# Optimization experiments

Hardware: AMD Instinct MI355X
Metric: run time of the kernel (lower is better)

The kernel has to match this reference:

```python
import jax, jax.numpy as jnp
import numpy as np

BS, E = 32, 4096  # BS fixed by repeat_interleave(32) in the source


def setup_inputs() -> dict:
    key = jax.random.key(0)
    ks = jax.random.split(key, 8)
    s = lambda k, shape, scale=0.02: jax.random.normal(k, shape, dtype=jnp.float32) * scale
    return {
        "image_features": jax.random.normal(ks[0], (BS, E), dtype=jnp.float32),
        "text_features": jax.random.normal(ks[1], (BS, E), dtype=jnp.float32),
        # fusion: BN(2E) -> ReLU -> Linear(2E,E)
        "fs_bn_g": jnp.ones((2 * E,), jnp.float32),
        "fs_bn_b": jnp.zeros((2 * E,), jnp.float32),
        "fs_w": s(ks[2], (2 * E, E)),
        "fs_b": jnp.zeros((E,), jnp.float32),
        # gating: Linear(E,E) -> BN -> ReLU -> Linear(E,E) -> Sigmoid
        "gt_w1": s(ks[3], (E, E)),
        "gt_b1": jnp.zeros((E,), jnp.float32),
        "gt_bn_g": jnp.ones((E,), jnp.float32),
        "gt_bn_b": jnp.zeros((E,), jnp.float32),
        "gt_w2": s(ks[4], (E, E)),
        "gt_b2": jnp.zeros((E,), jnp.float32),
        # 3 error-encoding blocks: Linear(E,E/2)->BN->ReLU->Linear(E/2,E)+residual
        "ee_w1": s(ks[5], (3, E, E // 2)),
        "ee_b1": jnp.zeros((3, E // 2), jnp.float32),
        "ee_bn_g": jnp.ones((3, E // 2), jnp.float32),
        "ee_bn_b": jnp.zeros((3, E // 2), jnp.float32),
        "ee_w2": s(ks[6], (3, E // 2, E)),
        "ee_b2": jnp.zeros((3, E), jnp.float32),
        "cell_id": 1,
    }


def _bn(x, g, b, eps=1e-5):
    # training-mode BatchNorm1d: per-call batch statistics (biased variance)
    mu = jnp.mean(x, axis=0, keepdims=True)
    var = jnp.mean((x - mu) ** 2, axis=0, keepdims=True)
    return (x - mu) * jax.lax.rsqrt(var + eps) * g + b


def reference(image_features, text_features, fs_bn_g, fs_bn_b, fs_w, fs_b,
              gt_w1, gt_b1, gt_bn_g, gt_bn_b, gt_w2, gt_b2,
              ee_w1, ee_b1, ee_bn_g, ee_bn_b, ee_w2, ee_b2, cell_id):
    # cell_id != 0 branch: the per-sample Python loop is vectorized with vmap.
    def compose(txt_row):  # txt_row: [E] -> tiled to [BS, E] (repeat_interleave of [1,E])
        t = jnp.broadcast_to(txt_row[None, :], image_features.shape)
        x = jnp.concatenate([image_features, t], axis=1)          # [BS, 2E]
        f = jax.nn.relu(_bn(x, fs_bn_g, fs_bn_b)) @ fs_w + fs_b   # fusion -> [BS, E]
        g = jax.nn.sigmoid(
            jax.nn.relu(_bn(f @ gt_w1 + gt_b1, gt_bn_g, gt_bn_b)) @ gt_w2 + gt_b2
        )                                                          # gating -> [BS, E]
        ff = f
        for i in range(3):  # structurally distinct error-encoding blocks
            h = jax.nn.relu(_bn(ff @ ee_w1[i] + ee_b1[i], ee_bn_g[i], ee_bn_b[i]))
            ff = h @ ee_w2[i] + ee_b2[i] + ff                      # residual
        return image_features * g + ff * (1.0 - g)                # [BS, E]

    return jax.vmap(compose)(text_features)                        # [BS, BS, E]
```

## Files before the change

kernel.cpp:

```cpp
#include <hip/hip_runtime.h>
#include <math.h>

#define EDIM 4096
#define BS 32
#define NT 64
#define KSPLIT 4
#define NWAVES 4
#define BLK 256

__device__ __forceinline__ float relu_f(float x) { return x > 0.f ? x : 0.f; }

__global__ void __launch_bounds__(BLK) prep_kernel(
    const float* __restrict__ img, const float* __restrict__ bng,
    const float* __restrict__ bnb, float* __restrict__ act0,
    float* __restrict__ vvec, int* __restrict__ flag)
{
  int n = blockIdx.x * BLK + threadIdx.x;
  float bv = bnb[EDIM + n];
  float vv = relu_f(bv);
  vvec[n] = vv;
  if (vv != 0.f) atomicOr(flag, 1);

  float s = 0.f, s2 = 0.f;
  for (int r = 0; r < BS; ++r) {
    float x = img[(size_t)r * EDIM + n];
    s += x; s2 += x * x;
  }
  float mean = s * (1.f / BS);
  float var  = s2 * (1.f / BS) - mean * mean;
  float sc = bng[n] * rsqrtf(var + 1e-5f);
  float sh = bnb[n] - mean * sc;
  for (int r = 0; r < BS; ++r) {
    float x = img[(size_t)r * EDIM + n];
    act0[(size_t)n * BS + r] = relu_f(x * sc + sh);
  }
}

__global__ void __launch_bounds__(BLK) mm_stage(
    const float* __restrict__ W, const float* __restrict__ Ain,
    const float* __restrict__ bias,
    const float* __restrict__ bng, const float* __restrict__ bnb,
    const float* __restrict__ res,
    const float* __restrict__ Wlow, const float* __restrict__ vvec,
    const int* __restrict__ flag,
    float* __restrict__ acc, int* __restrict__ counter,
    float* __restrict__ dst,
    int K, int N, int mode)
{
  const int tid  = threadIdx.x;
  const int bx   = blockIdx.x;
  const int tile = bx >> 2;
  const int ks   = bx & (KSPLIT - 1);
  const int wv   = __builtin_amdgcn_readfirstlane(tid >> 6);
  const int lane = tid & 63;
  const int n    = tile * NT + lane;
  const int kchunk = K / (KSPLIT * NWAVES);
  const int k0     = (ks * NWAVES + wv) * kchunk;

  float racc[BS];
#pragma unroll
  for (int r = 0; r < BS; ++r) racc[r] = 0.f;

  const float* wp = W + (size_t)k0 * N + n;
  const float* ap = Ain + (size_t)k0 * BS;

#pragma unroll 4
  for (int k = 0; k < kchunk; ++k) {
    float wval = wp[(size_t)k * N];
    const float* arow = ap + (size_t)k * BS;
#pragma unroll
    for (int r = 0; r < BS; ++r) racc[r] = fmaf(arow[r], wval, racc[r]);
  }

  if (Wlow != nullptr) {
    if (*flag) {
      float cpart = 0.f;
      const float* wl = Wlow + (size_t)k0 * N + n;
      for (int k = 0; k < kchunk; ++k)
        cpart = fmaf(vvec[k0 + k], wl[(size_t)k * N], cpart);
#pragma unroll
      for (int r = 0; r < BS; ++r) racc[r] += cpart;
    }
  }

  __shared__ float sred[NWAVES][NT][BS];
#pragma unroll
  for (int r = 0; r < BS; r += 4)
    *(float4*)&sred[wv][lane][r] = make_float4(racc[r], racc[r+1], racc[r+2], racc[r+3]);
  __syncthreads();

  const int c  = tid >> 2;
  const int rb = (tid & 3) * 8;
  float tot[8];
#pragma unroll
  for (int u = 0; u < 8; ++u)
    tot[u] = sred[0][c][rb+u] + sred[1][c][rb+u] + sred[2][c][rb+u] + sred[3][c][rb+u];

  const int col = tile * NT + c;
  float* ga = acc + (size_t)col * BS + rb;
#pragma unroll
  for (int u = 0; u < 8; ++u) atomicAdd(ga + u, tot[u]);

  __threadfence();
  __syncthreads();
  __shared__ int s_last;
  if (tid == 0) {
    int old = atomicAdd(counter + tile, 1);
    s_last = (old == KSPLIT - 1) ? 1 : 0;
  }
  __syncthreads();
  if (!s_last) return;

  float val[8];
#pragma unroll
  for (int u = 0; u < 8; ++u)
    val[u] = __hip_atomic_load(ga + u, __ATOMIC_RELAXED, __HIP_MEMORY_SCOPE_AGENT);

  const float bb = bias[col];
#pragma unroll
  for (int u = 0; u < 8; ++u) val[u] += bb;

  if (mode == 1) {
    __shared__ float sps[NT][4], sps2[NT][4], ssc[NT], ssh[NT];
    float p = 0.f, p2 = 0.f;
#pragma unroll
    for (int u = 0; u < 8; ++u) { p += val[u]; p2 += val[u] * val[u]; }
    sps[c][tid & 3] = p; sps2[c][tid & 3] = p2;
    __syncthreads();
    if (tid < NT) {
      float s  = sps[tid][0] + sps[tid][1] + sps[tid][2] + sps[tid][3];
      float s2 = sps2[tid][0] + sps2[tid][1] + sps2[tid][2] + sps2[tid][3];
      float mean = s * (1.f / BS);
      float var  = s2 * (1.f / BS) - mean * mean;
      float sc = bng[tile * NT + tid] * rsqrtf(var + 1e-5f);
      ssc[tid] = sc;
      ssh[tid] = bnb[tile * NT + tid] - mean * sc;
    }
    __syncthreads();
    float sc = ssc[c], sh = ssh[c];
    float* dp = dst + (size_t)col * BS + rb;
#pragma unroll
    for (int u = 0; u < 8; ++u) dp[u] = relu_f(val[u] * sc + sh);
  } else if (mode == 2) {
#pragma unroll
    for (int u = 0; u < 8; ++u) {
      float g = 1.f / (1.f + __expf(-val[u]));
      dst[(size_t)(rb + u) * EDIM + col] = g;
    }
  } else if (mode == 3) {
    const float* rp = res + (size_t)col * BS + rb;
    float* dp = dst + (size_t)col * BS + rb;
#pragma unroll
    for (int u = 0; u < 8; ++u) dp[u] = val[u] + rp[u];
  } else {
    float* dp = dst + (size_t)col * BS + rb;
#pragma unroll
    for (int u = 0; u < 8; ++u) dp[u] = val[u];
  }
}

__global__ void __launch_bounds__(BLK) final_kernel(
    const float* __restrict__ img, const float* __restrict__ grm,
    const float* __restrict__ fft, float* __restrict__ out)
{
  __shared__ float sff[BS][NT];
  const int tid  = threadIdx.x;
  const int tile = blockIdx.x & 63;
  const int jg   = blockIdx.x >> 6;
  const int c  = tid >> 2;
  const int rb = (tid & 3) * 8;
  const float* src = fft + (size_t)(tile * NT + c) * BS + rb;
#pragma unroll
  for (int u = 0; u < 8; ++u) sff[rb + u][c] = src[u];
  __syncthreads();

  const int le = tid & 63, rg = tid >> 6;
  const int e  = tile * NT + le;
#pragma unroll
  for (int rr = 0; rr < 8; ++rr) {
    int r = rr * 4 + rg;
    float gv = grm[(size_t)r * EDIM + e];
    float iv = img[(size_t)r * EDIM + e];
    float o  = iv * gv + sff[r][le] * (1.f - gv);
#pragma unroll
    for (int jj = 0; jj < 8; ++jj) {
      int j = jg * 8 + jj;
      out[((size_t)(j * BS + r)) * EDIM + e] = o;
    }
  }
}

extern "C" void kernel_launch(void* const* d_in, const int* in_sizes, int n_in,
                              void* d_out, int out_size, void* d_ws, size_t ws_size,
                              hipStream_t stream)
{
  const float* img    = (const float*)d_in[0];
  const float* fs_bng = (const float*)d_in[2];
  const float* fs_bnb = (const float*)d_in[3];
  const float* fs_w   = (const float*)d_in[4];
  const float* fs_b   = (const float*)d_in[5];
  const float* gt_w1  = (const float*)d_in[6];
  const float* gt_b1  = (const float*)d_in[7];
  const float* gt_bng = (const float*)d_in[8];
  const float* gt_bnb = (const float*)d_in[9];
  const float* gt_w2  = (const float*)d_in[10];
  const float* gt_b2  = (const float*)d_in[11];
  const float* ee_w1  = (const float*)d_in[12];
  const float* ee_b1  = (const float*)d_in[13];
  const float* ee_bng = (const float*)d_in[14];
  const float* ee_bnb = (const float*)d_in[15];
  const float* ee_w2  = (const float*)d_in[16];
  const float* ee_b2  = (const float*)d_in[17];
  float* out = (float*)d_out;

  float* w = (float*)d_ws;
  size_t o = 0;
  float* acc_fs = w + o; o += (size_t)EDIM * BS;
  float* acc_g1 = w + o; o += (size_t)EDIM * BS;
  float* acc_g2 = w + o; o += (size_t)EDIM * BS;
  float* acc_ea[3]; for (int i = 0; i < 3; ++i) { acc_ea[i] = w + o; o += (size_t)(EDIM/2) * BS; }
  float* acc_eb[3]; for (int i = 0; i < 3; ++i) { acc_eb[i] = w + o; o += (size_t)EDIM * BS; }
  int* counters = (int*)(w + o); o += 1024;
  int* flag = counters + 960;
  size_t zero_bytes = o * sizeof(float);
  float* act0 = w + o; o += (size_t)EDIM * BS;
  float* vvec = w + o; o += EDIM;
  float* fbuf = w + o; o += (size_t)EDIM * BS;
  float* hgb  = w + o; o += (size_t)EDIM * BS;
  float* gbuf = w + o; o += (size_t)EDIM * BS;
  float* he[3];  for (int i = 0; i < 3; ++i) { he[i]  = w + o; o += (size_t)(EDIM/2) * BS; }
  float* ffb[3]; for (int i = 0; i < 3; ++i) { ffb[i] = w + o; o += (size_t)EDIM * BS; }

  hipMemsetAsync(d_ws, 0, zero_bytes, stream);

  prep_kernel<<<EDIM / BLK, BLK, 0, stream>>>(img, fs_bng, fs_bnb, act0, vvec, flag);

  mm_stage<<<(EDIM / NT) * KSPLIT, BLK, 0, stream>>>(
      fs_w, act0, fs_b, nullptr, nullptr, nullptr,
      fs_w + (size_t)EDIM * EDIM, vvec, flag,
      acc_fs, counters + 0, fbuf, EDIM, EDIM, 0);

  mm_stage<<<(EDIM / NT) * KSPLIT, BLK, 0, stream>>>(
      gt_w1, fbuf, gt_b1, gt_bng, gt_bnb, nullptr, nullptr, nullptr, nullptr,
      acc_g1, counters + 64, hgb, EDIM, EDIM, 1);
  mm_stage<<<(EDIM / NT) * KSPLIT, BLK, 0, stream>>>(
      gt_w2, hgb, gt_b2, nullptr, nullptr, nullptr, nullptr, nullptr, nullptr,
      acc_g2, counters + 128, gbuf, EDIM, EDIM, 2);

  const float* ffin = fbuf;
  for (int i = 0; i < 3; ++i) {
    mm_stage<<<((EDIM / 2) / NT) * KSPLIT, BLK, 0, stream>>>(
        ee_w1 + (size_t)i * EDIM * (EDIM / 2), ffin,
        ee_b1 + (size_t)i * (EDIM / 2), ee_bng + (size_t)i * (EDIM / 2),
        ee_bnb + (size_t)i * (EDIM / 2),
        nullptr, nullptr, nullptr, nullptr,
        acc_ea[i], counters + 192 + i * 128, he[i], EDIM, EDIM / 2, 1);
    mm_stage<<<(EDIM / NT) * KSPLIT, BLK, 0, stream>>>(
        ee_w2 + (size_t)i * (EDIM / 2) * EDIM, he[i],
        ee_b2 + (size_t)i * EDIM, nullptr, nullptr, ffin,
        nullptr, nullptr, nullptr,
        acc_eb[i], counters + 256 + i * 128, ffb[i], EDIM / 2, EDIM, 3);
    ffin = ffb[i];
  }

  final_kernel<<<64 * 4, BLK, 0, stream>>>(img, gbuf, ffin, out);
}
```

Before: 889.6 us.

## Restructure GEMM stages with two-column float2 tiles and deeper split-K

The matrix stage kernel now has each lane own two adjacent output columns, loaded as float2, and reads the activation row as float4. Each block covers 128 columns, and split-K is raised to 16 or 32 so the grid becomes much larger. Partial sums go to the global accumulator in row-major order, and the last-arriving block finishes the whole column, including the batchnorm statistics. The aim is to fill more CUs and cut load instructions on this weight-bandwidth-bound skinny GEMM, at the cost of more global atomics.

```diff
diff --git a/kernel.cpp b/kernel.cpp
--- a/kernel.cpp
+++ b/kernel.cpp
@@ -3,9 +3,9 @@
 
 #define EDIM 4096
 #define BS 32
-#define NT 64
-#define KSPLIT 4
-#define NWAVES 4
+#define CPL 2
+#define COLS 128
+#define KWAVES 4
 #define BLK 256
 
 __device__ __forceinline__ float relu_f(float x) { return x > 0.f ? x : 0.f; }
@@ -36,126 +36,130 @@
   }
 }
 
-__global__ void __launch_bounds__(BLK) mm_stage(
+__global__ void __launch_bounds__(BLK, 2) mm_stage2(
     const float* __restrict__ W, const float* __restrict__ Ain,
     const float* __restrict__ bias,
     const float* __restrict__ bng, const float* __restrict__ bnb,
     const float* __restrict__ res,
     const float* __restrict__ Wlow, const float* __restrict__ vvec,
     const int* __restrict__ flag,
-    float* __restrict__ acc, int* __restrict__ counter,
+    float* __restrict__ gacc, int* __restrict__ counter,
     float* __restrict__ dst,
-    int K, int N, int mode)
+    int K, int N, int KS, int mode)
 {
   const int tid  = threadIdx.x;
-  const int bx   = blockIdx.x;
-  const int tile = bx >> 2;
-  const int ks   = bx & (KSPLIT - 1);
-  const int wv   = __builtin_amdgcn_readfirstlane(tid >> 6);
   const int lane = tid & 63;
-  const int n    = tile * NT + lane;
-  const int kchunk = K / (KSPLIT * NWAVES);
-  const int k0     = (ks * NWAVES + wv) * kchunk;
-
-  float racc[BS];
-#pragma unroll
-  for (int r = 0; r < BS; ++r) racc[r] = 0.f;
-
-  const float* wp = W + (size_t)k0 * N + n;
+  const int wv   = tid >> 6;
+  const int ncg  = N / COLS;
+  const int colgroup = blockIdx.x % ncg;
+  const int ks       = blockIdx.x / ncg;
+  const int kchunk = K / (KS * KWAVES);
+  const int k0     = (ks * KWAVES + wv) * kchunk;
+  const int n0     = colgroup * COLS + lane * CPL;
+
+  float2 acc[BS];
+#pragma unroll
+  for (int r = 0; r < BS; ++r) acc[r] = make_float2(0.f, 0.f);
+
+  const float* wp = W + (size_t)k0 * N + n0;
   const float* ap = Ain + (size_t)k0 * BS;
+
+#define ROWFMA(r, av) do { acc[r].x = fmaf((av), w.x, acc[r].x); \
+                           acc[r].y = fmaf((av), w.y, acc[r].y); } while (0)
 
 #pragma unroll 4
   for (int k = 0; k < kchunk; ++k) {
-    float wval = wp[(size_t)k * N];
-    const float* arow = ap + (size_t)k * BS;
-#pragma unroll
-    for (int r = 0; r < BS; ++r) racc[r] = fmaf(arow[r], wval, racc[r]);
-  }
+    float2 w = *(const float2*)(wp + (size_t)k * N);
+    const float4* ar = (const float4*)(ap + (size_t)k * BS);
+#pragma unroll
+    for (int rq = 0; rq < 8; ++rq) {
+      float4 a = ar[rq];
+      ROWFMA(rq * 4 + 0, a.x);
+      ROWFMA(rq * 4 + 1, a.y);
+      ROWFMA(rq * 4 + 2, a.z);
+      ROWFMA(rq * 4 + 3, a.w);
+    }
+  }
+#undef ROWFMA
 
   if (Wlow != nullptr) {
     if (*flag) {
-      float cpart = 0.f;
-      const float* wl = Wlow + (size_t)k0 * N + n;
-      for (int k = 0; k < kchunk; ++k)
-        cpart = fmaf(vvec[k0 + k], wl[(size_t)k * N], cpart);
-#pragma unroll
-      for (int r = 0; r < BS; ++r) racc[r] += cpart;
-    }
-  }
-
-  __shared__ float sred[NWAVES][NT][BS];
-#pragma unroll
-  for (int r = 0; r < BS; r += 4)
-    *(float4*)&sred[wv][lane][r] = make_float4(racc[r], racc[r+1], racc[r+2], racc[r+3]);
-  __syncthreads();
-
-  const int c  = tid >> 2;
-  const int rb = (tid & 3) * 8;
-  float tot[8];
-#pragma unroll
-  for (int u = 0; u < 8; ++u)
-    tot[u] = sred[0][c][rb+u] + sred[1][c][rb+u] + sred[2][c][rb+u] + sred[3][c][rb+u];
-
-  const int col = tile * NT + c;
-  float* ga = acc + (size_t)col * BS + rb;
-#pragma unroll
-  for (int u = 0; u < 8; ++u) atomicAdd(ga + u, tot[u]);
+      float2 cp = make_float2(0.f, 0.f);
+      const float* wl = Wlow + (size_t)k0 * N + n0;
+      for (int k = 0; k < kchunk; ++k) {
+        float vvk = vvec[k0 + k];
+        float2 w = *(const float2*)(wl + (size_t)k * N);
+        cp.x = fmaf(vvk, w.x, cp.x);
+        cp.y = fmaf(vvk, w.y, cp.y);
+      }
+#pragma unroll
+      for (int r = 0; r < BS; ++r) { acc[r].x += cp.x; acc[r].y += cp.y; }
+    }
+  }
+
+  __shared__ float sred[KWAVES][16][COLS];
+  const int rc = tid & (COLS - 1);
+  const int rbase = (tid >> 7) * 8;
+#pragma unroll
+  for (int p = 0; p < 2; ++p) {
+    if (p) __syncthreads();
+#pragma unroll
+    for (int r = 0; r < 16; ++r)
+      *(float2*)&sred[wv][r][lane * CPL] = acc[p * 16 + r];
+    __syncthreads();
+#pragma unroll
+    for (int i = 0; i < 8; ++i) {
+      int r = rbase + i;
+      float s = sred[0][r][rc] + sred[1][r][rc] + sred[2][r][rc] + sred[3][r][rc];
+      atomicAdd(&gacc[(size_t)(p * 16 + r) * N + colgroup * COLS + rc], s);
+    }
+  }
 
   __threadfence();
-  __syncthreads();
   __shared__ int s_last;
   if (tid == 0) {
-    int old = atomicAdd(counter + tile, 1);
-    s_last = (old == KSPLIT - 1) ? 1 : 0;
+    int old = atomicAdd(counter + colgroup, 1);
+    s_last = (old == KS - 1) ? 1 : 0;
   }
   __syncthreads();
   if (!s_last) return;
 
-  float val[8];
-#pragma unroll
-  for (int u = 0; u < 8; ++u)
-    val[u] = __hip_atomic_load(ga + u, __ATOMIC_RELAXED, __HIP_MEMORY_SCOPE_AGENT);
-
-  const float bb = bias[col];
-#pragma unroll
-  for (int u = 0; u < 8; ++u) val[u] += bb;
-
-  if (mode == 1) {
-    __shared__ float sps[NT][4], sps2[NT][4], ssc[NT], ssh[NT];
-    float p = 0.f, p2 = 0.f;
-#pragma unroll
-    for (int u = 0; u < 8; ++u) { p += val[u]; p2 += val[u] * val[u]; }
-    sps[c][tid & 3] = p; sps2[c][tid & 3] = p2;
-    __syncthreads();
-    if (tid < NT) {
-      float s  = sps[tid][0] + sps[tid][1] + sps[tid][2] + sps[tid][3];
-      float s2 = sps2[tid][0] + sps2[tid][1] + sps2[tid][2] + sps2[tid][3];
+  if (tid < COLS) {
+    const int n = colgroup * COLS + tid;
+    float val[BS];
+#pragma unroll
+    for (int r = 0; r < BS; ++r)
+      val[r] = __hip_atomic_load(&gacc[(size_t)r * N + n],
+                                 __ATOMIC_RELAXED, __HIP_MEMORY_SCOPE_AGENT);
+    const float bb = bias[n];
+#pragma unroll
+    for (int r = 0; r < BS; ++r) val[r] += bb;
+
+    if (mode == 1) {
+      float s = 0.f, s2 = 0.f;
+#pragma unroll
+      for (int r = 0; r < BS; ++r) { s += val[r]; s2 += val[r] * val[r]; }
       float mean = s * (1.f / BS);
       float var  = s2 * (1.f / BS) - mean * mean;
-      float sc = bng[tile * NT + tid] * rsqrtf(var + 1e-5f);
-      ssc[tid] = sc;
-      ssh[tid] = bnb[tile * NT + tid] - mean * sc;
-    }
-    __syncthreads();
-    float sc = ssc[c], sh = ssh[c];
-    float* dp = dst + (size_t)col * BS + rb;
-#pragma unroll
-    for (int u = 0; u < 8; ++u) dp[u] = relu_f(val[u] * sc + sh);
-  } else if (mode == 2) {
-#pragma unroll
-    for (int u = 0; u < 8; ++u) {
-      float g = 1.f / (1.f + __expf(-val[u]));
-      dst[(size_t)(rb + u) * EDIM + col] = g;
-    }
-  } else if (mode == 3) {
-    const float* rp = res + (size_t)col * BS + rb;
-    float* dp = dst + (size_t)col * BS + rb;
-#pragma unroll
-    for (int u = 0; u < 8; ++u) dp[u] = val[u] + rp[u];
-  } else {
-    float* dp = dst + (size_t)col * BS + rb;
-#pragma unroll
-    for (int u = 0; u < 8; ++u) dp[u] = val[u];
+      float sc = bng[n] * rsqrtf(var + 1e-5f);
+      float sh = bnb[n] - mean * sc;
+      float* dp = dst + (size_t)n * BS;
+#pragma unroll
+      for (int r = 0; r < BS; ++r) dp[r] = relu_f(val[r] * sc + sh);
+    } else if (mode == 2) {
+#pragma unroll
+      for (int r = 0; r < BS; ++r)
+        dst[(size_t)r * EDIM + n] = 1.f / (1.f + __expf(-val[r]));
+    } else if (mode == 3) {
+      const float* rp = res + (size_t)n * BS;
+      float* dp = dst + (size_t)n * BS;
+#pragma unroll
+      for (int r = 0; r < BS; ++r) dp[r] = val[r] + rp[r];
+    } else {
+      float* dp = dst + (size_t)n * BS;
+#pragma unroll
+      for (int r = 0; r < BS; ++r) dp[r] = val[r];
+    }
   }
 }
 
@@ -163,19 +167,19 @@
     const float* __restrict__ img, const float* __restrict__ grm,
     const float* __restrict__ fft, float* __restrict__ out)
 {
-  __shared__ float sff[BS][NT];
+  __shared__ float sff[BS][64];
   const int tid  = threadIdx.x;
   const int tile = blockIdx.x & 63;
   const int jg   = blockIdx.x >> 6;
   const int c  = tid >> 2;
   const int rb = (tid & 3) * 8;
-  const float* src = fft + (size_t)(tile * NT + c) * BS + rb;
+  const float* src = fft + (size_t)(tile * 64 + c) * BS + rb;
 #pragma unroll
   for (int u = 0; u < 8; ++u) sff[rb + u][c] = src[u];
   __syncthreads();
 
   const int le = tid & 63, rg = tid >> 6;
-  const int e  = tile * NT + le;
+  const int e  = tile * 64 + le;
 #pragma unroll
   for (int rr = 0; rr < 8; ++rr) {
     int r = rr * 4 + rg;
@@ -235,31 +239,34 @@
 
   prep_kernel<<<EDIM / BLK, BLK, 0, stream>>>(img, fs_bng, fs_bnb, act0, vvec, flag);
 
-  mm_stage<<<(EDIM / NT) * KSPLIT, BLK, 0, stream>>>(
+  const int KS_BIG = 16;
+  const int KS_EE1 = 32;
+
+  mm_stage2<<<(EDIM / COLS) * KS_BIG, BLK, 0, stream>>>(
       fs_w, act0, fs_b, nullptr, nullptr, nullptr,
       fs_w + (size_t)EDIM * EDIM, vvec, flag,
-      acc_fs, counters + 0, fbuf, EDIM, EDIM, 0);
-
-  mm_stage<<<(EDIM / NT) * KSPLIT, BLK, 0, stream>>>(
+      acc_fs, counters + 0, fbuf, EDIM, EDIM, KS_BIG, 0);
+
+  mm_stage2<<<(EDIM / COLS) * KS_BIG, BLK, 0, stream>>>(
       gt_w1, fbuf, gt_b1, gt_bng, gt_bnb, nullptr, nullptr, nullptr, nullptr,
-      acc_g1, counters + 64, hgb, EDIM, EDIM, 1);
-  mm_stage<<<(EDIM / NT) * KSPLIT, BLK, 0, stream>>>(
+      acc_g1, counters + 64, hgb, EDIM, EDIM, KS_BIG, 1);
+  mm_stage2<<<(EDIM / COLS) * KS_BIG, BLK, 0, stream>>>(
       gt_w2, hgb, gt_b2, nullptr, nullptr, nullptr, nullptr, nullptr, nullptr,
-      acc_g2, counters + 128, gbuf, EDIM, EDIM, 2);
+      acc_g2, counters + 128, gbuf, EDIM, EDIM, KS_BIG, 2);
 
   const float* ffin = fbuf;
   for (int i = 0; i < 3; ++i) {
-    mm_stage<<<((EDIM / 2) / NT) * KSPLIT, BLK, 0, stream>>>(
+    mm_stage2<<<((EDIM / 2) / COLS) * KS_EE1, BLK, 0, stream>>>(
         ee_w1 + (size_t)i * EDIM * (EDIM / 2), ffin,
         ee_b1 + (size_t)i * (EDIM / 2), ee_bng + (size_t)i * (EDIM / 2),
         ee_bnb + (size_t)i * (EDIM / 2),
         nullptr, nullptr, nullptr, nullptr,
-        acc_ea[i], counters + 192 + i * 128, he[i], EDIM, EDIM / 2, 1);
-    mm_stage<<<(EDIM / NT) * KSPLIT, BLK, 0, stream>>>(
+        acc_ea[i], counters + 192 + i * 128, he[i], EDIM, EDIM / 2, KS_EE1, 1);
+    mm_stage2<<<(EDIM / COLS) * KS_BIG, BLK, 0, stream>>>(
         ee_w2 + (size_t)i * (EDIM / 2) * EDIM, he[i],
         ee_b2 + (size_t)i * EDIM, nullptr, nullptr, ffin,
         nullptr, nullptr, nullptr,
-        acc_eb[i], counters + 256 + i * 128, ffb[i], EDIM / 2, EDIM, 3);
+        acc_eb[i], counters + 256 + i * 128, ffb[i], EDIM / 2, EDIM, KS_BIG, 3);
     ffin = ffb[i];
   }
 
```

Result: slower. 1.068 ms (+20.0%).
